# Kernel tuning notes

Hardware: AMD Instinct MI355X
Metric: run time of the kernel (lower is better)

## Reference

```python
import jax, jax.numpy as jnp
import numpy as np

D_MODEL = 1024
N_HEADS = 16
D_K = 64  # per-head dim and the scaling denominator used by the module
NEG = -1e9  # stand-in for -inf in masked_fill (rows are never fully masked)


def setup_inputs() -> dict:
    key = jax.random.key(0)
    ks = jax.random.split(key, 8)
    B, M, N = 2, 2048, 2048
    q = jax.random.normal(ks[0], (B, M, D_MODEL), dtype=jnp.float32)
    k = jax.random.normal(ks[1], (B, N, D_MODEL), dtype=jnp.float32)
    v = jax.random.normal(ks[2], (B, N, D_MODEL), dtype=jnp.float32)
    mask = jax.random.randint(ks[3], (B, M, N), 0, 2).astype(jnp.bool_)
    # xavier_uniform for square [d,d] weights: limit = sqrt(6/(d+d))
    lim = float(np.sqrt(6.0 / (D_MODEL + D_MODEL)))
    Wq = jax.random.uniform(ks[4], (D_MODEL, D_MODEL), jnp.float32, -lim, lim)
    Wk = jax.random.uniform(ks[5], (D_MODEL, D_MODEL), jnp.float32, -lim, lim)
    Wv = jax.random.uniform(ks[6], (D_MODEL, D_MODEL), jnp.float32, -lim, lim)
    Wo = jax.random.uniform(ks[7], (D_MODEL, D_MODEL), jnp.float32, -lim, lim)
    return {"q": q, "k": k, "v": v, "mask": mask,
            "Wq": Wq, "Wk": Wk, "Wv": Wv, "Wo": Wo}


def _split_heads(x):
    # (B, S, D) -> (B, H, S, Dh); the torch split/cat-on-batch trick is
    # mathematically identical to this standard head reshape.
    B, S, _ = x.shape
    return x.reshape(B, S, N_HEADS, D_K).transpose(0, 2, 1, 3)


def reference(q, k, v, mask, Wq, Wk, Wv, Wo):
    qw = _split_heads(q @ Wq.T)  # (B,H,M,Dh)
    kw = _split_heads(k @ Wk.T)  # (B,H,N,Dh)
    vw = _split_heads(v @ Wv.T)  # (B,H,N,Dh)
    scores = jnp.einsum('bhmd,bhnd->bhmn', qw, kw)
    scores = jnp.where(mask[:, None, :, :], NEG, scores)
    attn = jax.nn.softmax(scores / jnp.sqrt(jnp.float32(D_K)), axis=-1)
    ctx = jnp.einsum('bhmn,bhnd->bhmd', attn, vw)
    B, _, M, _ = ctx.shape
    ctx = ctx.transpose(0, 2, 1, 3).reshape(B, M, D_MODEL)
    return ctx @ Wo.T
```

## Files before the change

kernel.cpp:

```cpp
#include <hip/hip_runtime.h>
#include <hip/hip_bf16.h>
#include <stdint.h>
#include <string.h>

#define SEQ   2048
#define DM    1024
#define NH    16
#define NB    2

typedef __attribute__((ext_vector_type(8))) short bf16x8;
typedef __attribute__((ext_vector_type(4))) float f32x4;
typedef unsigned short u16;
typedef unsigned int   u32;

__device__ __forceinline__ u16 f2bf(float f) {
    u32 u = __float_as_uint(f);
    u += 0x7FFF + ((u >> 16) & 1);
    return (u16)(u >> 16);
}
__device__ __forceinline__ u32 pk2bf(float a, float b) {
    __hip_bfloat162 p = __float22bfloat162_rn(make_float2(a, b));
    u32 u; memcpy(&u, &p, 4); return u;
}
__device__ __forceinline__ float fexp2(float x) {
#if __has_builtin(__builtin_amdgcn_exp2f)
    return __builtin_amdgcn_exp2f(x);
#else
    return exp2f(x);
#endif
}
__device__ __forceinline__ float mask_exp2(float s, u32 lsel, int pos) {
#if __has_builtin(__builtin_amdgcn_sbfe)
    u32 keep = (u32)__builtin_amdgcn_sbfe((int)lsel, pos, 1);
#else
    u32 keep = (u32)((int)(lsel << (31 - pos)) >> 31);
#endif
    return __uint_as_float(__float_as_uint(fexp2(s)) & keep);
}
__device__ __forceinline__ void gl_lds16(const void* g, void* l) {
    __builtin_amdgcn_global_load_lds(
        (const __attribute__((address_space(1))) u32*)g,
        (__attribute__((address_space(3))) u32*)l, 16, 0, 0);
}
__device__ __forceinline__ void wbar_vm3() { asm volatile("s_waitcnt vmcnt(3)\ns_barrier" ::: "memory"); }
__device__ __forceinline__ void wbar_vm4() { asm volatile("s_waitcnt vmcnt(4)\ns_barrier" ::: "memory"); }
__device__ __forceinline__ void vm_drain() { asm volatile("s_waitcnt vmcnt(0)" ::: "memory"); }

struct CvtArgs {
    const float* s[7];
    u16* d[7];
    float scale[7];
    int start[8];
    const int* mask;
    u32* mbits;
};
__global__ __launch_bounds__(256) void cvt_kernel(CvtArgs a) {
    int bid = blockIdx.x;
    int tid = threadIdx.x;
    if (bid >= 8192) {
        int widx = (bid - 8192) * 256 + tid;
        uint4 v = ((const uint4*)a.mask)[widx];
        unsigned long long b0 = __ballot(v.x != 0);
        unsigned long long b1 = __ballot(v.y != 0);
        unsigned long long b2 = __ballot(v.z != 0);
        unsigned long long b3 = __ballot(v.w != 0);
        int lane = tid & 63;
        if (lane < 4) {
            int sh = lane * 16;
            u32 lo = (u32)((b0 >> sh) & 0xFFFF) | ((u32)((b1 >> sh) & 0xFFFF) << 16);
            u32 hi = (u32)((b2 >> sh) & 0xFFFF) | ((u32)((b3 >> sh) & 0xFFFF) << 16);
            size_t N = (size_t)(bid - 8192) * 1024 + (size_t)(tid >> 6) * 256
                     + (size_t)lane * 64;
            u32* dst = a.mbits + ((N >> 11) * 64 + ((N >> 6) & 31) * 2);
            *(uint2*)dst = make_uint2(lo, hi);
        }
        return;
    }
    int seg = 0;
#pragma unroll
    for (int i = 1; i < 7; ++i) if (bid >= a.start[i]) seg = i;
    float sc = a.scale[seg];
    size_t base = (size_t)(bid - a.start[seg]) * 2048 + tid * 8;
    const float4* s4 = (const float4*)(a.s[seg] + base);
    float4 x = s4[0], y = s4[1];
    u32 r[4];
    r[0] = pk2bf(x.x*sc, x.y*sc); r[1] = pk2bf(x.z*sc, x.w*sc);
    r[2] = pk2bf(y.x*sc, y.y*sc); r[3] = pk2bf(y.z*sc, y.w*sc);
    *(uint4*)(a.d[seg] + base) = *(uint4*)r;
}

template<int RT>
__device__ __forceinline__ void gemm_body(const u16* __restrict__ A,
                                          const u16* __restrict__ Bm,
                                          void* __restrict__ Y,
                                          int rtile, int ctile, int mode,
                                          u16* sA, u16* sB) {
    constexpr int ABUF = RT * 32 * 32;
    constexpr int BBUF = 128 * 32;
    const int tid  = threadIdx.x;
    const int wv   = tid >> 6, lane = tid & 63;
    const int quad = lane >> 4, ln = lane & 15;
    const int wr   = wv >> 1,  wc  = wv & 1;

    const int lr4 = lane >> 2;
    const int lcc = ((lane & 3) ^ ((lane >> 3) & 3)) * 8;

    const u16* gA[RT/2]; u16* lA[RT/2];
#pragma unroll
    for (int s = 0; s < RT/2; ++s) {
        int seg = wv * (RT/2) + s;
        gA[s] = A + (size_t)(rtile * (RT*32) + seg*16 + lr4) * 1024 + lcc;
        lA[s] = sA + seg * 512;
    }
    const u16* gB[2]; u16* lB[2];
#pragma unroll
    for (int s = 0; s < 2; ++s) {
        int seg = wv * 2 + s;
        gB[s] = Bm + (size_t)(ctile * 128 + seg*16 + lr4) * 1024 + lcc;
        lB[s] = sB + seg * 512;
    }

    f32x4 acc[RT][4];
#pragma unroll
    for (int i = 0; i < RT; ++i)
#pragma unroll
        for (int j = 0; j < 4; ++j) acc[i][j] = (f32x4){0.f,0.f,0.f,0.f};

    const int c0 = (quad ^ ((ln >> 1) & 3)) * 8;

#pragma unroll
    for (int s = 0; s < RT/2; ++s) gl_lds16(gA[s], lA[s]);
#pragma unroll
    for (int s = 0; s < 2; ++s)    gl_lds16(gB[s], lB[s]);
#pragma unroll
    for (int s = 0; s < RT/2; ++s) gl_lds16(gA[s] + 32, lA[s] + ABUF);
#pragma unroll
    for (int s = 0; s < 2; ++s)    gl_lds16(gB[s] + 32, lB[s] + BBUF);

    int bc = 0, bp = 2;
    for (int kt = 0; kt < 32; ++kt) {
        if (RT == 4) wbar_vm4(); else wbar_vm3();
        int pk = (kt + 2) & 31;
#pragma unroll
        for (int s = 0; s < RT/2; ++s) gl_lds16(gA[s] + pk*32, lA[s] + bp*ABUF);
#pragma unroll
        for (int s = 0; s < 2; ++s)    gl_lds16(gB[s] + pk*32, lB[s] + bp*BBUF);

        const u16* sAb = sA + bc * ABUF;
        const u16* sBb = sB + bc * BBUF;
        bf16x8 af[RT], bfr[4];
#pragma unroll
        for (int rt = 0; rt < RT; ++rt)
            af[rt] = *(const bf16x8*)(sAb + (wr*(RT*16) + rt*16 + ln) * 32 + c0);
#pragma unroll
        for (int ct = 0; ct < 4; ++ct)
            bfr[ct] = *(const bf16x8*)(sBb + (wc*64 + ct*16 + ln) * 32 + c0);
#pragma unroll
        for (int rt = 0; rt < RT; ++rt)
#pragma unroll
            for (int ct = 0; ct < 4; ++ct)
                acc[rt][ct] = __builtin_amdgcn_mfma_f32_16x16x32_bf16(
                    af[rt], bfr[ct], acc[rt][ct], 0, 0, 0);

        bc = (bc == 2) ? 0 : bc + 1;
        bp = (bp == 2) ? 0 : bp + 1;
    }
    vm_drain();

#pragma unroll
    for (int rt = 0; rt < RT; ++rt) {
#pragma unroll
        for (int ct = 0; ct < 4; ++ct) {
#pragma unroll
            for (int i = 0; i < 4; ++i) {
                int R = rtile*(RT*32) + wr*(RT*16) + rt*16 + quad*4 + i;
                int C = ctile*128 + wc*64 + ct*16 + ln;
                float val = acc[rt][ct][i];
                if (mode == 0) {
                    int b = R >> 11, s = R & 2047, h = C >> 6, d = C & 63;
                    ((u16*)Y)[((size_t)((b*NH + h) * SEQ + s) << 6) + d] = f2bf(val);
                } else if (mode == 1) {
                    int h = R >> 6, d = R & 63, b = C >> 11, n = C & 2047;
                    int nl = n & 63;
                    int np = (nl & 32) | (((nl & 15) >> 2) << 3) | (nl & 3)
                           | ((nl & 16) >> 2);
                    n = (n & ~63) | np;
                    ((u16*)Y)[((size_t)((b*NH + h) * 64 + d) << 11) + n] = f2bf(val);
                } else {
                    ((float*)Y)[(size_t)R * 1024 + C] = val;
                }
            }
        }
    }
}

struct QKVArgs { const u16* A[3]; const u16* B[3]; u16* Y[3]; };

__global__ __launch_bounds__(256) void gemm_qkv(QKVArgs g) {
    __shared__ u16 sA[3 * 128 * 32];
    __shared__ u16 sB[3 * 128 * 32];
    int z = blockIdx.z;
    if (z == 2)
        gemm_body<4>(g.A[2], g.B[2], g.Y[2], blockIdx.y, blockIdx.x, 1, sA, sB);
    else
        gemm_body<4>(g.A[z], g.B[z], g.Y[z], blockIdx.x, blockIdx.y, 0, sA, sB);
}

__global__ __launch_bounds__(256) void gemm_out(const u16* __restrict__ A,
                                                const u16* __restrict__ Bm,
                                                float* __restrict__ Y) {
    __shared__ u16 sA[3 * 64 * 32];
    __shared__ u16 sB[3 * 128 * 32];
    gemm_body<2>(A, Bm, Y, blockIdx.x, blockIdx.y, 2, sA, sB);
}

__global__ __launch_bounds__(512, 4) void attn_kernel(
    const u16* __restrict__ qw,
    const u16* __restrict__ kw,
    const u16* __restrict__ vt,
    const u32* __restrict__ mbits,
    u16* __restrict__ ctx) {

    __shared__ __align__(16) u16 smem[32768];
    u16* sK = smem;
    u16* sV = smem + 16384;

    const int mtile = blockIdx.x;
    const int bh    = blockIdx.y;
    const int b     = bh >> 4;
    const int tid   = threadIdx.x;
    const int wv    = tid >> 6, lane = tid & 63;
    const int quad  = lane >> 4, ln = lane & 15;
    const int g     = wv >> 2;
    const int w2    = wv & 3;
    const int m0    = mtile * 128;

    const size_t hbase = (size_t)bh * SEQ * 64;

    bf16x8 qf[2][2];
#pragma unroll
    for (int mt = 0; mt < 2; ++mt) {
        const u16* qp = qw + hbase + (size_t)(m0 + w2*32 + mt*16 + ln) * 64 + quad*8;
        qf[mt][0] = *(const bf16x8*)(qp);
        qf[mt][1] = *(const bf16x8*)(qp + 32);
    }

    f32x4 o[2][4], lsum[2];
#pragma unroll
    for (int mt = 0; mt < 2; ++mt) {
        lsum[mt] = (f32x4){0.f,0.f,0.f,0.f};
#pragma unroll
        for (int j = 0; j < 4; ++j) o[mt][j] = (f32x4){0.f,0.f,0.f,0.f};
    }

    bf16x8 ones;
#pragma unroll
    for (int i = 0; i < 8; ++i) ones[i] = (short)0x3F80;

    const u32* mrow0 = mbits + (size_t)(b*SEQ + m0 + w2*32 + ln) * 64;
    const u32* mrow1 = mrow0 + ((size_t)16 * 64);

    const int lr = lane >> 3;
    const int lc = (lane & 7) ^ lr;
    const u16* gK = kw + hbase + (size_t)(wv*8 + lr) * 64 + lc*8;
    const u16* gV = vt + hbase + (size_t)(wv*8 + lr) * SEQ + lc*8;
    u16* lK = sK + wv * 512;
    u16* lV = sV + wv * 512;

    const int c0 = (quad ^ (ln & 7)) * 8;
    const u16* a1 = smem + ln*64 + c0;
    const u16* a2 = smem + ln*64 + (c0 ^ 32);
    const u16* aK1 = a1 + g*2048;
    const u16* aK2 = a2 + g*2048;
    const u16* aV  = (g ? a2 : a1) + 16384;
    const int  msh = g*8 + quad;

    gl_lds16(gK, lK);
    gl_lds16(gV, lV);
    uint2 wA0 = *(const uint2*)(mrow0);
    uint2 wA1 = *(const uint2*)(mrow1);
    gl_lds16(gK + 4096, lK + 4096);
    gl_lds16(gV + 64,   lV + 4096);
    uint2 wB0 = *(const uint2*)(mrow0 + 2);
    uint2 wB1 = *(const uint2*)(mrow1 + 2);

    for (int mi = 0; mi < 8; ++mi) {
#pragma unroll
        for (int u = 0; u < 4; ++u) {
            const int bc = u;
            const int wb = (u + 2) & 3;
            wbar_vm4();
            int pidx = (mi*4 + u + 2) & 31;
            gl_lds16(gK + (size_t)pidx * 4096, lK + wb*4096);
            gl_lds16(gV + pidx * 64,           lV + wb*4096);
            uint2 wC0 = *(const uint2*)(mrow0 + pidx*2);
            uint2 wC1 = *(const uint2*)(mrow1 + pidx*2);

            f32x4 s4[2][2];
            __builtin_amdgcn_s_setprio(1);
#pragma unroll
            for (int ct2 = 0; ct2 < 2; ++ct2) {
                bf16x8 k0 = *(const bf16x8*)(aK1 + bc*4096 + ct2*1024);
                bf16x8 k1 = *(const bf16x8*)(aK2 + bc*4096 + ct2*1024);
#pragma unroll
                for (int mt = 0; mt < 2; ++mt) {
                    f32x4 z = (f32x4){0.f, 0.f, 0.f, 0.f};
                    z = __builtin_amdgcn_mfma_f32_16x16x32_bf16(k0, qf[mt][0], z, 0, 0, 0);
                    z = __builtin_amdgcn_mfma_f32_16x16x32_bf16(k1, qf[mt][1], z, 0, 0, 0);
                    s4[mt][ct2] = z;
                }
            }
            __builtin_amdgcn_s_setprio(0);

            bf16x8 pfm[2];
#pragma unroll
            for (int mt = 0; mt < 2; ++mt) {
                u32 wx = mt ? wA1.x : wA0.x;
                u32 wy = mt ? wA1.y : wA0.y;
                u32 l0 = ~(wx >> msh);
                u32 l1 = ~(wy >> msh);
                u32 P[4];
#pragma unroll
                for (int ct2 = 0; ct2 < 2; ++ct2) {
                    float p[4];
                    p[0] = mask_exp2(s4[mt][ct2][0], l0, ct2*4);
                    p[1] = mask_exp2(s4[mt][ct2][1], l0, 16 + ct2*4);
                    p[2] = mask_exp2(s4[mt][ct2][2], l1, ct2*4);
                    p[3] = mask_exp2(s4[mt][ct2][3], l1, 16 + ct2*4);
                    P[ct2*2]     = pk2bf(p[0], p[1]);
                    P[ct2*2 + 1] = pk2bf(p[2], p[3]);
                }
                memcpy(&pfm[mt], P, 16);
            }

            __builtin_amdgcn_s_setprio(1);
            lsum[0] = __builtin_amdgcn_mfma_f32_16x16x32_bf16(pfm[0], ones, lsum[0], 0, 0, 0);
            lsum[1] = __builtin_amdgcn_mfma_f32_16x16x32_bf16(pfm[1], ones, lsum[1], 0, 0, 0);
#pragma unroll
            for (int ct = 0; ct < 4; ++ct) {
                bf16x8 vf = *(const bf16x8*)(aV + bc*4096 + ct*1024);
                o[0][ct] = __builtin_amdgcn_mfma_f32_16x16x32_bf16(pfm[0], vf, o[0][ct], 0, 0, 0);
                o[1][ct] = __builtin_amdgcn_mfma_f32_16x16x32_bf16(pfm[1], vf, o[1][ct], 0, 0, 0);
            }
            __builtin_amdgcn_s_setprio(0);

            wA0 = wB0; wA1 = wB1;
            wB0 = wC0; wB1 = wC1;
        }
    }
    vm_drain();
    __syncthreads();

    float* sO  = (float*)smem;
    float* sLs = (float*)((char*)smem + 34816);
    if (g == 1) {
#pragma unroll
        for (int mt = 0; mt < 2; ++mt)
#pragma unroll
            for (int i = 0; i < 4; ++i) {
                int lm = w2*32 + mt*16 + quad*4 + i;
                sLs[lm] = lsum[mt][i];
#pragma unroll
                for (int ct = 0; ct < 4; ++ct)
                    sO[lm*68 + ct*16 + ln] = o[mt][ct][i];
            }
    }
    __syncthreads();
    if (g == 0) {
#pragma unroll
        for (int mt = 0; mt < 2; ++mt)
#pragma unroll
            for (int i = 0; i < 4; ++i) {
                int lm = w2*32 + mt*16 + quad*4 + i;
                float inv = 1.f / (lsum[mt][i] + sLs[lm]);
                int m = m0 + lm;
                size_t base = ((size_t)(b * SEQ + m) << 10) + (bh & 15) * 64;
#pragma unroll
                for (int ct = 0; ct < 4; ++ct)
                    ctx[base + ct*16 + ln] =
                        f2bf((o[mt][ct][i] + sO[lm*68 + ct*16 + ln]) * inv);
            }
    }
}

extern "C" void kernel_launch(void* const* d_in, const int* in_sizes, int n_in,
                              void* d_out, int out_size, void* d_ws, size_t ws_size,
                              hipStream_t stream) {
    const float* q    = (const float*)d_in[0];
    const float* k    = (const float*)d_in[1];
    const float* v    = (const float*)d_in[2];
    const int*   mask = (const int*)d_in[3];
    const float* Wq   = (const float*)d_in[4];
    const float* Wk   = (const float*)d_in[5];
    const float* Wv   = (const float*)d_in[6];
    const float* Wo   = (const float*)d_in[7];
    float* out = (float*)d_out;

    char* ws = (char*)d_ws;
    const size_t SZH = (size_t)NB * SEQ * DM * 2;
    const size_t SZW = (size_t)DM * DM * 2;
    u16* qw   = (u16*)(ws);
    u16* kw   = (u16*)(ws + SZH);
    u16* vt   = (u16*)(ws + 2*SZH);
    u16* ctx  = (u16*)(ws + 3*SZH);
    u16* vb   = ctx;
    u32* mbits= (u32*)(ws + 4*SZH);
    u16* qb   = (u16*)(ws + 4*SZH + (1u<<20));
    u16* kb   = (u16*)(ws + 4*SZH + (1u<<20) + SZH);
    u16* Wqb  = (u16*)(ws + 4*SZH + (1u<<20) + 2*SZH);
    u16* Wkb  = (u16*)((char*)Wqb + SZW);
    u16* Wvb  = (u16*)((char*)Wqb + 2*SZW);
    u16* Wob  = (u16*)((char*)Wqb + 3*SZW);

    const float CSC = 0.18033688011112042f;

    CvtArgs ca;
    ca.s[0]=q;  ca.d[0]=qb;  ca.scale[0]=1.f;
    ca.s[1]=k;  ca.d[1]=kb;  ca.scale[1]=1.f;
    ca.s[2]=v;  ca.d[2]=vb;  ca.scale[2]=1.f;
    ca.s[3]=Wq; ca.d[3]=Wqb; ca.scale[3]=CSC;
    ca.s[4]=Wk; ca.d[4]=Wkb; ca.scale[4]=1.f;
    ca.s[5]=Wv; ca.d[5]=Wvb; ca.scale[5]=1.f;
    ca.s[6]=Wo; ca.d[6]=Wob; ca.scale[6]=1.f;
    int st[8] = {0, 2048, 4096, 6144, 6656, 7168, 7680, 8192};
    for (int i = 0; i < 8; ++i) ca.start[i] = st[i];
    ca.mask  = mask;
    ca.mbits = mbits;
    cvt_kernel<<<dim3(16384), dim3(256), 0, stream>>>(ca);

    QKVArgs ga;
    ga.A[0]=qb;  ga.B[0]=Wqb; ga.Y[0]=qw;
    ga.A[1]=kb;  ga.B[1]=Wkb; ga.Y[1]=kw;
    ga.A[2]=Wvb; ga.B[2]=vb;  ga.Y[2]=vt;
    gemm_qkv<<<dim3(32, 8, 3), dim3(256), 0, stream>>>(ga);

    attn_kernel<<<dim3(SEQ/128, NB*NH), dim3(512), 0, stream>>>(qw, kw, vt, mbits, ctx);

    gemm_out<<<dim3(64, 8), dim3(256), 0, stream>>>(ctx, Wob, out);
}
```

Measured before the change: 251.2 us.

## Replace QKV projection GEMM with 256x256-tile, 512-thread double-buffered kernel

The QKV projection moves from a 128x128-tile, 256-thread GEMM to a dedicated 256x256-tile kernel with 8 waves, a 64-wide K step and double-buffered XOR-swizzled LDS filled by direct global-to-LDS loads. Each wave computes a 128x64 sub-tile, which raises MFMA work per byte loaded and reuses A fragments across four B column groups. The grid drops to 192 blocks with 128KB of LDS each. That may leave some of the 256 CUs idle and limit occupancy, trading parallelism for better reuse. A variable rename in the attention kernel is cosmetic.

```diff
diff --git a/kernel.cpp b/kernel.cpp
--- a/kernel.cpp
+++ b/kernel.cpp
@@ -42,8 +42,10 @@
         (const __attribute__((address_space(1))) u32*)g,
         (__attribute__((address_space(3))) u32*)l, 16, 0, 0);
 }
+__device__ __forceinline__ void wbar_vm2() { asm volatile("s_waitcnt vmcnt(2)\ns_barrier" ::: "memory"); }
 __device__ __forceinline__ void wbar_vm3() { asm volatile("s_waitcnt vmcnt(3)\ns_barrier" ::: "memory"); }
 __device__ __forceinline__ void wbar_vm4() { asm volatile("s_waitcnt vmcnt(4)\ns_barrier" ::: "memory"); }
+__device__ __forceinline__ void bar()      { asm volatile("s_barrier" ::: "memory"); }
 __device__ __forceinline__ void vm_drain() { asm volatile("s_waitcnt vmcnt(0)" ::: "memory"); }
 
 struct CvtArgs {
@@ -196,14 +198,106 @@
 
 struct QKVArgs { const u16* A[3]; const u16* B[3]; u16* Y[3]; };
 
-__global__ __launch_bounds__(256) void gemm_qkv(QKVArgs g) {
-    __shared__ u16 sA[3 * 128 * 32];
-    __shared__ u16 sB[3 * 128 * 32];
-    int z = blockIdx.z;
-    if (z == 2)
-        gemm_body<4>(g.A[2], g.B[2], g.Y[2], blockIdx.y, blockIdx.x, 1, sA, sB);
-    else
-        gemm_body<4>(g.A[z], g.B[z], g.Y[z], blockIdx.x, blockIdx.y, 0, sA, sB);
+__global__ __launch_bounds__(512, 2) void gemm_qkv256(QKVArgs g) {
+    __shared__ __align__(16) u16 smem[65536];
+
+    const int z  = blockIdx.y;
+    const int bx = blockIdx.x;
+    int rtile, ctile, mode;
+    if (z == 2) { rtile = bx & 3;  ctile = bx >> 2; mode = 1; }
+    else        { rtile = bx >> 2; ctile = bx & 3;  mode = 0; }
+    const u16* Aa = g.A[z];
+    const u16* Ba = g.B[z];
+    u16*       Yy = g.Y[z];
+
+    const int tid  = threadIdx.x;
+    const int wv   = tid >> 6, lane = tid & 63;
+    const int quad = lane >> 4, ln = lane & 15;
+    const int wr   = wv >> 2,  wc  = wv & 3;
+
+    const int r0  = tid >> 3;
+    const int lcq = ((tid & 7) ^ (r0 & 7)) * 8;
+    const u16* srcs[4];
+    srcs[0] = Aa + (size_t)(rtile*256 +       r0) * 1024 + lcq;
+    srcs[1] = Aa + (size_t)(rtile*256 + 128 + r0) * 1024 + lcq;
+    srcs[2] = Ba + (size_t)(ctile*256 +       r0) * 1024 + lcq;
+    srcs[3] = Ba + (size_t)(ctile*256 + 128 + r0) * 1024 + lcq;
+
+    const int sw3 = (ln & 7) << 3;
+    const int cs0 = (quad * 8) ^ sw3;
+    const int cs1 = (32 + quad * 8) ^ sw3;
+    const u16* aA  = smem + wr*8192 + ln*64 + cs0;
+    const u16* aA2 = smem + wr*8192 + ln*64 + cs1;
+    const u16* bB  = smem + 16384 + (wc>>1)*8192 + (wc&1)*4096 + ln*64 + cs0;
+    const u16* bB2 = smem + 16384 + (wc>>1)*8192 + (wc&1)*4096 + ln*64 + cs1;
+
+    f32x4 acc[8][4];
+#pragma unroll
+    for (int i = 0; i < 8; ++i)
+#pragma unroll
+        for (int j = 0; j < 4; ++j) acc[i][j] = (f32x4){0.f,0.f,0.f,0.f};
+
+#pragma unroll
+    for (int p = 0; p < 4; ++p) {
+        u16* dst = smem + p*8192 + wv*512;
+        gl_lds16(srcs[p], dst);
+        gl_lds16(srcs[p] + 65536, dst + 4096);
+    }
+
+    for (int kt = 0; kt < 16; ++kt) {
+        const int D  = (kt & 1) << 15;
+        const int Dp = D ^ 32768;
+        const int pk = (kt + 1) & 15;
+        bf16x8 af[8][2];
+#pragma unroll
+        for (int p = 0; p < 4; ++p) {
+            u16* dst = smem + Dp + p*8192 + wv*512;
+            gl_lds16(srcs[p] + pk*64, dst);
+            gl_lds16(srcs[p] + pk*64 + 65536, dst + 4096);
+            if (p == 0) wbar_vm2(); else bar();
+            if (p == 0) {
+#pragma unroll
+                for (int mf = 0; mf < 8; ++mf) {
+                    af[mf][0] = *(const bf16x8*)(aA  + D + mf*1024);
+                    af[mf][1] = *(const bf16x8*)(aA2 + D + mf*1024);
+                }
+            }
+            bf16x8 b0 = *(const bf16x8*)(bB  + D + p*1024);
+            bf16x8 b1 = *(const bf16x8*)(bB2 + D + p*1024);
+            __builtin_amdgcn_s_setprio(1);
+#pragma unroll
+            for (int mf = 0; mf < 8; ++mf) {
+                acc[mf][p] = __builtin_amdgcn_mfma_f32_16x16x32_bf16(
+                    af[mf][0], b0, acc[mf][p], 0, 0, 0);
+                acc[mf][p] = __builtin_amdgcn_mfma_f32_16x16x32_bf16(
+                    af[mf][1], b1, acc[mf][p], 0, 0, 0);
+            }
+            __builtin_amdgcn_s_setprio(0);
+        }
+    }
+    vm_drain();
+
+#pragma unroll
+    for (int mf = 0; mf < 8; ++mf)
+#pragma unroll
+        for (int nf = 0; nf < 4; ++nf)
+#pragma unroll
+            for (int i = 0; i < 4; ++i) {
+                int R = rtile*256 + wr*128 + mf*16 + quad*4 + i;
+                int C = ctile*256 + wc*64 + nf*16 + ln;
+                float val = acc[mf][nf][i];
+                if (mode == 0) {
+                    int b = R >> 11, s = R & 2047, h = C >> 6, d = C & 63;
+                    Yy[((size_t)((b*NH + h) * SEQ + s) << 6) + d] = f2bf(val);
+                } else {
+                    int h = R >> 6, d = R & 63, b = C >> 11, n = C & 2047;
+                    int nl = n & 63;
+                    int np = (nl & 32) | (((nl & 15) >> 2) << 3) | (nl & 3)
+                           | ((nl & 16) >> 2);
+                    n = (n & ~63) | np;
+                    Yy[((size_t)((b*NH + h) * 64 + d) << 11) + n] = f2bf(val);
+                }
+            }
 }
 
 __global__ __launch_bounds__(256) void gemm_out(const u16* __restrict__ A,
@@ -304,10 +398,10 @@
                 bf16x8 k1 = *(const bf16x8*)(aK2 + bc*4096 + ct2*1024);
 #pragma unroll
                 for (int mt = 0; mt < 2; ++mt) {
-                    f32x4 z = (f32x4){0.f, 0.f, 0.f, 0.f};
-                    z = __builtin_amdgcn_mfma_f32_16x16x32_bf16(k0, qf[mt][0], z, 0, 0, 0);
-                    z = __builtin_amdgcn_mfma_f32_16x16x32_bf16(k1, qf[mt][1], z, 0, 0, 0);
-                    s4[mt][ct2] = z;
+                    f32x4 zz = (f32x4){0.f, 0.f, 0.f, 0.f};
+                    zz = __builtin_amdgcn_mfma_f32_16x16x32_bf16(k0, qf[mt][0], zz, 0, 0, 0);
+                    zz = __builtin_amdgcn_mfma_f32_16x16x32_bf16(k1, qf[mt][1], zz, 0, 0, 0);
+                    s4[mt][ct2] = zz;
                 }
             }
             __builtin_amdgcn_s_setprio(0);
@@ -432,7 +526,7 @@
     ga.A[0]=qb;  ga.B[0]=Wqb; ga.Y[0]=qw;
     ga.A[1]=kb;  ga.B[1]=Wkb; ga.Y[1]=kw;
     ga.A[2]=Wvb; ga.B[2]=vb;  ga.Y[2]=vt;
-    gemm_qkv<<<dim3(32, 8, 3), dim3(256), 0, stream>>>(ga);
+    gemm_qkv256<<<dim3(64, 3), dim3(512), 0, stream>>>(ga);
 
     attn_kernel<<<dim3(SEQ/128, NB*NH), dim3(512), 0, stream>>>(qw, kw, vt, mbits, ctx);
 
```

Result: faster. 245.5 us (-2.2%).
